# Performance work log

Hardware: AMD Instinct MI355X
Metric: run time of the kernel (lower is better)

## Reference

```python
import jax, jax.numpy as jnp
import numpy as np

K = 7  # kernel_size


def setup_inputs() -> dict:
    key = jax.random.key(0)
    ks = jax.random.split(key, 7)
    B, C, H, W = 32, 256, 56, 56
    x = jax.random.normal(ks[0], (B, C, H, W), jnp.float32)
    # BatchNorm2d affine params
    bn_gamma = 1.0 + 0.1 * jax.random.normal(ks[1], (C,), jnp.float32)
    bn_beta = 0.1 * jax.random.normal(ks[2], (C,), jnp.float32)
    # Linear(k^2 -> k), torch weight layout (out, in)
    w0 = jax.random.normal(ks[3], (K, K * K), jnp.float32) / np.sqrt(K * K)
    # LayerNorm([C, k]) affine params
    ln_gamma = 1.0 + 0.1 * jax.random.normal(ks[4], (C, K), jnp.float32)
    ln_beta = 0.1 * jax.random.normal(ks[5], (C, K), jnp.float32)
    # Linear(k -> k^2)
    w1 = jax.random.normal(ks[6], (K * K, K), jnp.float32) / np.sqrt(K)
    return dict(x=x, bn_gamma=bn_gamma, bn_beta=bn_beta, w0=w0,
                ln_gamma=ln_gamma, ln_beta=ln_beta, w1=w1)


def reference(x, bn_gamma, bn_beta, w0, ln_gamma, ln_beta, w1):
    B, C, H, W = x.shape
    k = K
    eps = 1e-5
    # AdaptiveAvgPool2d((k,k)); H,W divisible by k -> exact block means
    p = x.reshape(B, C, k, H // k, k, W // k).mean(axis=(3, 5))  # (B,C,k,k)
    # BatchNorm2d (training-mode batch statistics, biased variance)
    mu = p.mean(axis=(0, 2, 3), keepdims=True)
    var = p.var(axis=(0, 2, 3), keepdims=True)
    p = (p - mu) * jax.lax.rsqrt(var + eps)
    p = p * bn_gamma[None, :, None, None] + bn_beta[None, :, None, None]
    # b c kh kw -> b c (kh kw), then Linear(k^2 -> k)
    v = p.reshape(B, C, k * k) @ w0.T  # (B,C,k)
    # LayerNorm over the (C,k) normalized shape
    m = v.mean(axis=(1, 2), keepdims=True)
    s = v.var(axis=(1, 2), keepdims=True)
    v = (v - m) * jax.lax.rsqrt(s + eps) * ln_gamma[None] + ln_beta[None]
    v = jax.nn.sigmoid(v)
    v = v @ w1.T  # (B,C,k^2)
    kern = v.reshape(B * C, 1, k, k)  # per-sample, per-channel depthwise kernels
    # F.conv2d(groups=B*C, padding='same', stride=1); odd k -> 'SAME' matches torch
    out = jax.lax.conv_general_dilated(
        x.reshape(1, B * C, H, W), kern,
        window_strides=(1, 1), padding='SAME',
        feature_group_count=B * C,
        dimension_numbers=('NCHW', 'OIHW', 'NCHW'))
    return out.reshape(B, C, H, W)
```

## Files before the change

### kernel.cpp

```cpp
#include <hip/hip_runtime.h>
#include <math.h>

#define BATCH 32
#define CH    256
#define HH    56
#define WW    56
#define HW    3136
#define KS    7
#define KK    49
#define NIMG  8192
#define PITCH 64
#define PROWS 62

__global__ __launch_bounds__(256) void pool_kernel(const float* __restrict__ x,
                                                   float* __restrict__ p) {
    __shared__ float tile[HW];
    const int img = blockIdx.x;
    const float* xi = x + (size_t)img * HW;
    for (int i = threadIdx.x; i < HW; i += 256) tile[i] = xi[i];
    __syncthreads();
    if (threadIdx.x < KK) {
        const int pr = threadIdx.x / KS, pc = threadIdx.x % KS;
        float s = 0.f;
        #pragma unroll
        for (int r = 0; r < 8; ++r) {
            const int base = (pr * 8 + r) * WW + pc * 8;
            #pragma unroll
            for (int c = 0; c < 8; ++c) s += tile[base + c];
        }
        p[(size_t)img * KK + threadIdx.x] = s * (1.0f / 64.0f);
    }
}

__global__ __launch_bounds__(256) void bnstats_kernel(const float* __restrict__ p,
                                                      const float* __restrict__ gamma,
                                                      const float* __restrict__ beta,
                                                      float* __restrict__ scale,
                                                      float* __restrict__ shift) {
    const int c = blockIdx.x;
    float s = 0.f, s2 = 0.f;
    for (int t = threadIdx.x; t < BATCH * KK; t += 256) {
        const int b = t / KK, i = t - b * KK;
        const float v = p[((size_t)b * CH + c) * KK + i];
        s += v; s2 += v * v;
    }
    #pragma unroll
    for (int o = 32; o >= 1; o >>= 1) {
        s  += __shfl_down(s, o, 64);
        s2 += __shfl_down(s2, o, 64);
    }
    __shared__ float r1[4], r2[4];
    const int w = threadIdx.x >> 6;
    if ((threadIdx.x & 63) == 0) { r1[w] = s; r2[w] = s2; }
    __syncthreads();
    if (threadIdx.x == 0) {
        const float S  = r1[0] + r1[1] + r1[2] + r1[3];
        const float S2 = r2[0] + r2[1] + r2[2] + r2[3];
        const float inv = 1.0f / (float)(BATCH * KK);
        const float mu  = S * inv;
        const float var = S2 * inv - mu * mu;
        const float rstd = rsqrtf(var + 1e-5f);
        const float sc = gamma[c] * rstd;
        scale[c] = sc;
        shift[c] = beta[c] - mu * sc;
    }
}

__global__ __launch_bounds__(256) void mid_kernel(const float* __restrict__ p,
                                                  const float* __restrict__ scale,
                                                  const float* __restrict__ shift,
                                                  const float* __restrict__ w0,
                                                  const float* __restrict__ lng,
                                                  const float* __restrict__ lnb,
                                                  const float* __restrict__ w1,
                                                  float* __restrict__ ker) {
    const int b = blockIdx.x, c = threadIdx.x;
    __shared__ float s_w0[KS * KK], s_w1[KK * KS];
    __shared__ float r1[4], r2[4];
    for (int i = threadIdx.x; i < KS * KK; i += 256) { s_w0[i] = w0[i]; s_w1[i] = w1[i]; }
    __syncthreads();
    float pn[KK];
    const float* pp = p + ((size_t)b * CH + c) * KK;
    const float sc = scale[c], sh = shift[c];
    #pragma unroll
    for (int i = 0; i < KK; ++i) pn[i] = pp[i] * sc + sh;
    float v[KS];
    float ls = 0.f, ls2 = 0.f;
    #pragma unroll
    for (int j = 0; j < KS; ++j) {
        float a = 0.f;
        #pragma unroll
        for (int i = 0; i < KK; ++i) a += pn[i] * s_w0[j * KK + i];
        v[j] = a; ls += a; ls2 += a * a;
    }
    #pragma unroll
    for (int o = 32; o >= 1; o >>= 1) {
        ls  += __shfl_down(ls, o, 64);
        ls2 += __shfl_down(ls2, o, 64);
    }
    const int w = threadIdx.x >> 6;
    if ((threadIdx.x & 63) == 0) { r1[w] = ls; r2[w] = ls2; }
    __syncthreads();
    const float S  = r1[0] + r1[1] + r1[2] + r1[3];
    const float S2 = r2[0] + r2[1] + r2[2] + r2[3];
    const float inv = 1.0f / (float)(CH * KS);
    const float m   = S * inv;
    const float var = S2 * inv - m * m;
    const float rs  = rsqrtf(var + 1e-5f);
    float sg[KS];
    #pragma unroll
    for (int j = 0; j < KS; ++j) {
        const float vn = (v[j] - m) * rs * lng[c * KS + j] + lnb[c * KS + j];
        sg[j] = 1.0f / (1.0f + expf(-vn));
    }
    float* ko = ker + ((size_t)b * CH + c) * KK;
    #pragma unroll
    for (int i = 0; i < KK; ++i) {
        float a = 0.f;
        #pragma unroll
        for (int j = 0; j < KS; ++j) a += sg[j] * s_w1[i * KS + j];
        ko[i] = a;
    }
}

__global__ __launch_bounds__(448) void conv_kernel(const float* __restrict__ x,
                                                   const float* __restrict__ ker,
                                                   float* __restrict__ out) {
    __shared__ float pad[PROWS * PITCH];
    __shared__ float kf[KK];
    const int img = blockIdx.x;
    const int t = threadIdx.x;
    const float* xi = x + (size_t)img * HW;
    if (t < KK) kf[t] = ker[(size_t)img * KK + t];
    for (int i = t; i < PROWS * PITCH; i += 448) {
        const int pr = i >> 6, pc = i & 63;
        const int r = pr - 3, c = pc - 3;
        float v = 0.f;
        if (r >= 0 && r < HH && c >= 0 && c < WW) v = xi[r * WW + c];
        pad[i] = v;
    }
    __syncthreads();
    const int col = t % 56;
    const int r0  = (t / 56) * 7;
    float acc[7] = {0.f, 0.f, 0.f, 0.f, 0.f, 0.f, 0.f};
    #pragma unroll
    for (int kw = 0; kw < 7; ++kw) {
        float wv[13];
        #pragma unroll
        for (int rr = 0; rr < 13; ++rr) wv[rr] = pad[(r0 + rr) * PITCH + col + kw];
        #pragma unroll
        for (int kr = 0; kr < 7; ++kr) {
            const float kv = kf[kr * 7 + kw];
            #pragma unroll
            for (int rr = 0; rr < 7; ++rr) acc[rr] += wv[rr + kr] * kv;
        }
    }
    float* oi = out + (size_t)img * HW;
    #pragma unroll
    for (int rr = 0; rr < 7; ++rr) oi[(r0 + rr) * WW + col] = acc[rr];
}

extern "C" void kernel_launch(void* const* d_in, const int* in_sizes, int n_in,
                              void* d_out, int out_size, void* d_ws, size_t ws_size,
                              hipStream_t stream) {
    const float* x   = (const float*)d_in[0];
    const float* bng = (const float*)d_in[1];
    const float* bnb = (const float*)d_in[2];
    const float* w0  = (const float*)d_in[3];
    const float* lng = (const float*)d_in[4];
    const float* lnb = (const float*)d_in[5];
    const float* w1  = (const float*)d_in[6];
    float* out = (float*)d_out;

    float* ws    = (float*)d_ws;
    float* p     = ws;
    float* scale = p + (size_t)NIMG * KK;
    float* shift = scale + CH;
    float* kern  = shift + CH;

    hipLaunchKernelGGL(pool_kernel,    dim3(NIMG),  dim3(256), 0, stream, x, p);
    hipLaunchKernelGGL(bnstats_kernel, dim3(CH),    dim3(256), 0, stream, p, bng, bnb, scale, shift);
    hipLaunchKernelGGL(mid_kernel,     dim3(BATCH), dim3(256), 0, stream, p, scale, shift,
                       w0, lng, lnb, w1, kern);
    hipLaunchKernelGGL(conv_kernel,    dim3(NIMG),  dim3(448), 0, stream, x, kern, out);
}
```

Measured before the change: 263.4 us.

## Register-tile depthwise conv with swizzled LDS and vectorize pooling loads

The pooling kernel stops staging each image in shared memory. Each thread now sums float4 columns over 8 rows straight from global memory, and a shuffle combines pairs of threads into one pooled value, with 4 images per block. The conv kernel processes 4 images per block, keeps all 49 weights in registers, and computes a 7x4 output tile per thread. It reads float4 rows from an XOR-swizzled padded shared buffer to cut bank conflicts and writes results as float4 stores. The costs are higher register pressure and about 62KB of LDS per block, which may lower occupancy.

```diff
diff --git a/kernel.cpp b/kernel.cpp
--- a/kernel.cpp
+++ b/kernel.cpp
@@ -11,25 +11,26 @@
 #define NIMG  8192
 #define PITCH 64
 #define PROWS 62
-
-__global__ __launch_bounds__(256) void pool_kernel(const float* __restrict__ x,
+#define PIMG  (PROWS*PITCH)
+#define IPB   4
+
+__global__ __launch_bounds__(392) void pool_kernel(const float* __restrict__ x,
                                                    float* __restrict__ p) {
-    __shared__ float tile[HW];
-    const int img = blockIdx.x;
-    const float* xi = x + (size_t)img * HW;
-    for (int i = threadIdx.x; i < HW; i += 256) tile[i] = xi[i];
-    __syncthreads();
-    if (threadIdx.x < KK) {
-        const int pr = threadIdx.x / KS, pc = threadIdx.x % KS;
-        float s = 0.f;
-        #pragma unroll
-        for (int r = 0; r < 8; ++r) {
-            const int base = (pr * 8 + r) * WW + pc * 8;
-            #pragma unroll
-            for (int c = 0; c < 8; ++c) s += tile[base + c];
-        }
-        p[(size_t)img * KK + threadIdx.x] = s * (1.0f / 64.0f);
-    }
+    const int t   = threadIdx.x;
+    const int im  = t / 98, rem = t % 98;
+    const int pr  = rem / 14, cq = rem % 14;
+    const int img = blockIdx.x * 4 + im;
+    const float4* xr = (const float4*)(x + (size_t)img * HW);
+    float4 s4 = make_float4(0.f, 0.f, 0.f, 0.f);
+    #pragma unroll
+    for (int r = 0; r < 8; ++r) {
+        const float4 v = xr[(pr * 8 + r) * 14 + cq];
+        s4.x += v.x; s4.y += v.y; s4.z += v.z; s4.w += v.w;
+    }
+    float s = (s4.x + s4.y) + (s4.z + s4.w);
+    s += __shfl_down(s, 1, 64);
+    if ((cq & 1) == 0)
+        p[(size_t)img * KK + pr * KS + (cq >> 1)] = s * (1.0f / 64.0f);
 }
 
 __global__ __launch_bounds__(256) void bnstats_kernel(const float* __restrict__ p,
@@ -126,38 +127,65 @@
 __global__ __launch_bounds__(448) void conv_kernel(const float* __restrict__ x,
                                                    const float* __restrict__ ker,
                                                    float* __restrict__ out) {
-    __shared__ float pad[PROWS * PITCH];
-    __shared__ float kf[KK];
-    const int img = blockIdx.x;
-    const int t = threadIdx.x;
-    const float* xi = x + (size_t)img * HW;
-    if (t < KK) kf[t] = ker[(size_t)img * KK + t];
-    for (int i = t; i < PROWS * PITCH; i += 448) {
-        const int pr = i >> 6, pc = i & 63;
-        const int r = pr - 3, c = pc - 3;
-        float v = 0.f;
-        if (r >= 0 && r < HH && c >= 0 && c < WW) v = xi[r * WW + c];
-        pad[i] = v;
-    }
-    __syncthreads();
-    const int col = t % 56;
-    const int r0  = (t / 56) * 7;
-    float acc[7] = {0.f, 0.f, 0.f, 0.f, 0.f, 0.f, 0.f};
-    #pragma unroll
-    for (int kw = 0; kw < 7; ++kw) {
-        float wv[13];
-        #pragma unroll
-        for (int rr = 0; rr < 13; ++rr) wv[rr] = pad[(r0 + rr) * PITCH + col + kw];
+    __shared__ __align__(16) float pad[IPB * PIMG];
+    __shared__ float kfl[IPB * KK];
+    const int t    = threadIdx.x;
+    const int img0 = blockIdx.x * IPB;
+    if (t < IPB * KK) kfl[t] = ker[(size_t)img0 * KK + t];
+    #pragma unroll
+    for (int imS = 0; imS < IPB; ++imS) {
+        const float* xi = x + (size_t)(img0 + imS) * HW;
+        float* pd = pad + imS * PIMG;
+        for (int i = t; i < PIMG; i += 448) {
+            const int prr = i >> 6, pcs = i & 63;
+            const int pc  = pcs ^ ((prr & 7) << 2);
+            const int r = prr - 3, cc = pc - 3;
+            float v = 0.f;
+            if ((unsigned)r < 56u && (unsigned)cc < 56u) v = xi[r * WW + cc];
+            pd[i] = v;
+        }
+    }
+    __syncthreads();
+    const int im  = t / 112, rem = t % 112;
+    const int cq  = rem % 14, st = rem / 14;
+    const int oc0 = cq * 4, orow0 = st * 7;
+    float kv[KK];
+    #pragma unroll
+    for (int i = 0; i < KK; ++i) kv[i] = kfl[im * KK + i];
+    float acc[7][4];
+    #pragma unroll
+    for (int a = 0; a < 7; ++a)
+        #pragma unroll
+        for (int d = 0; d < 4; ++d) acc[a][d] = 0.f;
+    const float* pd = pad + im * PIMG;
+    #pragma unroll
+    for (int ri = 0; ri < 13; ++ri) {
+        const int prr = orow0 + ri;
+        const int sw  = (prr & 7) << 2;
+        const float4 A = *(const float4*)&pd[prr * PITCH + ((oc0    ) ^ sw)];
+        const float4 B = *(const float4*)&pd[prr * PITCH + ((oc0 + 4) ^ sw)];
+        const float4 C = *(const float4*)&pd[prr * PITCH + ((oc0 + 8) ^ sw)];
+        const float w[12] = {A.x, A.y, A.z, A.w, B.x, B.y, B.z, B.w, C.x, C.y, C.z, C.w};
         #pragma unroll
         for (int kr = 0; kr < 7; ++kr) {
-            const float kv = kf[kr * 7 + kw];
+            const int orow = ri - kr;
+            if (orow < 0 || orow > 6) continue;
             #pragma unroll
-            for (int rr = 0; rr < 7; ++rr) acc[rr] += wv[rr + kr] * kv;
+            for (int kw = 0; kw < 7; ++kw) {
+                const float kvv = kv[kr * 7 + kw];
+                acc[orow][0] += w[kw    ] * kvv;
+                acc[orow][1] += w[kw + 1] * kvv;
+                acc[orow][2] += w[kw + 2] * kvv;
+                acc[orow][3] += w[kw + 3] * kvv;
+            }
         }
     }
-    float* oi = out + (size_t)img * HW;
-    #pragma unroll
-    for (int rr = 0; rr < 7; ++rr) oi[(r0 + rr) * WW + col] = acc[rr];
+    float* oi = out + (size_t)(img0 + im) * HW;
+    #pragma unroll
+    for (int rr = 0; rr < 7; ++rr) {
+        const float4 o4 = make_float4(acc[rr][0], acc[rr][1], acc[rr][2], acc[rr][3]);
+        *(float4*)&oi[(orow0 + rr) * WW + oc0] = o4;
+    }
 }
 
 extern "C" void kernel_launch(void* const* d_in, const int* in_sizes, int n_in,
@@ -178,9 +206,9 @@
     float* shift = scale + CH;
     float* kern  = shift + CH;
 
-    hipLaunchKernelGGL(pool_kernel,    dim3(NIMG),  dim3(256), 0, stream, x, p);
-    hipLaunchKernelGGL(bnstats_kernel, dim3(CH),    dim3(256), 0, stream, p, bng, bnb, scale, shift);
-    hipLaunchKernelGGL(mid_kernel,     dim3(BATCH), dim3(256), 0, stream, p, scale, shift,
+    hipLaunchKernelGGL(pool_kernel,    dim3(NIMG / 4), dim3(392), 0, stream, x, p);
+    hipLaunchKernelGGL(bnstats_kernel, dim3(CH),       dim3(256), 0, stream, p, bng, bnb, scale, shift);
+    hipLaunchKernelGGL(mid_kernel,     dim3(BATCH),    dim3(256), 0, stream, p, scale, shift,
                        w0, lng, lnb, w1, kern);
-    hipLaunchKernelGGL(conv_kernel,    dim3(NIMG),  dim3(448), 0, stream, x, kern, out);
-}
+    hipLaunchKernelGGL(conv_kernel,    dim3(NIMG / IPB), dim3(448), 0, stream, x, kern, out);
+}
```

Result: slower. 314.4 us (+19.4%).
